# Kernel tuning notes

Measured on AMD Instinct MI355X. Metric: run time of the kernel, lower is better.

The kernel has to match this reference:

```python
import jax, jax.numpy as jnp
import numpy as np

NUM_EXPERTS = 8
TOP_K = 2


def setup_inputs() -> dict:
    key = jax.random.key(0)
    k1, k2, k3, k4, k5 = jax.random.split(key, 5)
    B, S, H, F, E = 4, 2048, 1024, 4096, NUM_EXPERTS
    return {
        "hidden_states": jax.random.normal(k1, (B, S, H), dtype=jnp.float32),
        "gate_w": jax.random.normal(k2, (E, H), dtype=jnp.float32) * 0.02,
        "w1": jax.random.normal(k3, (E, F, H), dtype=jnp.float32) * 0.02,
        "w3": jax.random.normal(k4, (E, F, H), dtype=jnp.float32) * 0.02,
        "w2": jax.random.normal(k5, (E, H, F), dtype=jnp.float32) * 0.02,
    }


def reference(hidden_states, gate_w, w1, w3, w2):
    B, S, H = hidden_states.shape
    E = gate_w.shape[0]
    x = hidden_states.reshape(-1, H)  # [T, H]
    T = x.shape[0]

    # Router: logits -> fp32 softmax -> top-k -> renormalize (Mixtral)
    router_logits = x @ gate_w.T  # [T, E]
    probs = jax.nn.softmax(router_logits.astype(jnp.float32), axis=-1)
    top_w, top_idx = jax.lax.top_k(probs, TOP_K)  # [T, K]
    top_w = top_w / jnp.sum(top_w, axis=-1, keepdims=True)
    top_w = top_w.astype(x.dtype)

    # Combine weights per (token, expert); zero for unselected experts.
    comb = jnp.zeros((T, E), dtype=x.dtype).at[
        jnp.arange(T)[:, None], top_idx
    ].add(top_w)  # [T, E]

    out = jnp.zeros((T, H), dtype=x.dtype)
    for e in range(E):  # structural loop over distinct expert weights
        h = jax.nn.silu(x @ w1[e].T) * (x @ w3[e].T)  # [T, F]
        out = out + comb[:, e:e + 1] * (h @ w2[e].T)  # [T, H]

    return out.reshape(B, S, H), router_logits
```

## Files before the change

kernel.cpp:

```cpp
#include <hip/hip_runtime.h>
#include <hip/hip_bf16.h>
#include <stdint.h>

#define T_TOK 8192
#define H_DIM 1024
#define F_DIM 4096
#define NEXP  8
#define CAP        17408
#define CAP_TILES  136

typedef __attribute__((ext_vector_type(8))) short bf16x8;
typedef __attribute__((ext_vector_type(4))) float f32x4;

#define AS1 __attribute__((address_space(1)))
#define AS3 __attribute__((address_space(3)))

__device__ __forceinline__ void gload_lds16(const void* g, void* l) {
  __builtin_amdgcn_global_load_lds((const AS1 void*)g, (AS3 void*)l, 16, 0, 0);
}

struct TK { int i0, i1; float w0, w1; };

__global__ __launch_bounds__(256) void router_kernel(
    const float* __restrict__ x, const float* __restrict__ gw,
    float* __restrict__ logits, int* __restrict__ counts, TK* __restrict__ tk)
{
  const int lane = threadIdx.x & 63;
  const int t = blockIdx.x * 4 + (threadIdx.x >> 6);
  const float* xp = x + (size_t)t * H_DIM;
  float xr[16];
#pragma unroll
  for (int i = 0; i < 16; ++i) xr[i] = xp[lane + i * 64];
  float lg[NEXP];
#pragma unroll
  for (int e = 0; e < NEXP; ++e) {
    const float* gp = gw + e * H_DIM;
    float acc = 0.f;
#pragma unroll
    for (int i = 0; i < 16; ++i) acc += xr[i] * gp[lane + i * 64];
#pragma unroll
    for (int s = 32; s > 0; s >>= 1) acc += __shfl_xor(acc, s, 64);
    lg[e] = acc;
  }
  if (lane < NEXP) logits[(size_t)t * NEXP + lane] = lg[lane];
  if (lane == 0) {
    int i0 = 0; float m0 = lg[0];
#pragma unroll
    for (int e = 1; e < NEXP; ++e) if (lg[e] > m0) { m0 = lg[e]; i0 = e; }
    int i1 = -1; float m1 = -1e30f;
#pragma unroll
    for (int e = 0; e < NEXP; ++e) if (e != i0 && lg[e] > m1) { m1 = lg[e]; i1 = e; }
    float r = expf(m1 - m0);
    float w0 = 1.f / (1.f + r);
    float w1 = r / (1.f + r);
    TK v; v.i0 = i0; v.i1 = i1; v.w0 = w0; v.w1 = w1;
    tk[t] = v;
    atomicAdd(&counts[i0], 1);
    atomicAdd(&counts[i1], 1);
  }
}

__global__ void scan_kernel(const int* __restrict__ counts, int* __restrict__ offs,
                            int* __restrict__ cursor, int* __restrict__ tile_expert)
{
  if (threadIdx.x == 0 && blockIdx.x == 0) {
    int o = 0;
    for (int e = 0; e < NEXP; ++e) {
      offs[e] = o; cursor[e] = o;
      o += (counts[e] + 127) & ~127;
    }
    offs[NEXP] = o;
    for (int ti = 0; ti < CAP_TILES; ++ti) {
      int row = ti * 128;
      int e = NEXP - 1;
      for (int k = 0; k < NEXP; ++k)
        if (row >= offs[k] && row < offs[k + 1]) { e = k; break; }
      tile_expert[ti] = e;
    }
  }
}

__global__ __launch_bounds__(256) void scatter_kernel(
    const TK* __restrict__ tk, int* __restrict__ cursor,
    int* __restrict__ pair_tok, float* __restrict__ pair_w)
{
  int t = blockIdx.x * 256 + threadIdx.x;
  if (t >= T_TOK) return;
  TK v = tk[t];
  int p0 = atomicAdd(&cursor[v.i0], 1);
  pair_tok[p0] = t; pair_w[p0] = v.w0;
  int p1 = atomicAdd(&cursor[v.i1], 1);
  pair_tok[p1] = t; pair_w[p1] = v.w1;
}

union Pack8 { __hip_bfloat16 o[8]; uint4 u; };

__global__ __launch_bounds__(256) void gather_kernel(
    const float* __restrict__ x, const int* __restrict__ pair_tok,
    __hip_bfloat16* __restrict__ xg)
{
  int idx = blockIdx.x * 256 + threadIdx.x;
  int row = idx >> 7;
  int c8  = (idx & 127) << 3;
  int tok = pair_tok[row];
  const float4* src = reinterpret_cast<const float4*>(x + (size_t)tok * H_DIM + c8);
  float4 a = src[0], b = src[1];
  Pack8 pk;
  pk.o[0] = __float2bfloat16(a.x); pk.o[1] = __float2bfloat16(a.y);
  pk.o[2] = __float2bfloat16(a.z); pk.o[3] = __float2bfloat16(a.w);
  pk.o[4] = __float2bfloat16(b.x); pk.o[5] = __float2bfloat16(b.y);
  pk.o[6] = __float2bfloat16(b.z); pk.o[7] = __float2bfloat16(b.w);
  *reinterpret_cast<uint4*>(xg + (size_t)row * H_DIM + c8) = pk.u;
}

__global__ __launch_bounds__(256) void convert_kernel(
    const float* __restrict__ src, __hip_bfloat16* __restrict__ dst, long long n)
{
  long long i = ((long long)blockIdx.x * 256 + threadIdx.x) * 8;
  if (i >= n) return;
  float4 a = *reinterpret_cast<const float4*>(src + i);
  float4 b = *reinterpret_cast<const float4*>(src + i + 4);
  Pack8 pk;
  pk.o[0] = __float2bfloat16(a.x); pk.o[1] = __float2bfloat16(a.y);
  pk.o[2] = __float2bfloat16(a.z); pk.o[3] = __float2bfloat16(a.w);
  pk.o[4] = __float2bfloat16(b.x); pk.o[5] = __float2bfloat16(b.y);
  pk.o[6] = __float2bfloat16(b.z); pk.o[7] = __float2bfloat16(b.w);
  *reinterpret_cast<uint4*>(dst + i) = pk.u;
}

__global__ __launch_bounds__(256, 2) void gemm1_kernel(
    const __hip_bfloat16* __restrict__ xg,
    const __hip_bfloat16* __restrict__ w1b,
    const __hip_bfloat16* __restrict__ w3b,
    const int* __restrict__ tile_expert,
    __hip_bfloat16* __restrict__ h)
{
  __shared__ __hip_bfloat16 sA[128 * 32], sB1[128 * 32], sB3[128 * 32];
  const int tm = blockIdx.x;
  const int tf = blockIdx.y;
  const int e  = tile_expert[tm];
  const int tid = threadIdx.x;

  const __hip_bfloat16* A  = xg  + (size_t)tm * 128 * H_DIM;
  const __hip_bfloat16* B1 = w1b + (size_t)e * F_DIM * H_DIM + (size_t)tf * 128 * H_DIM;
  const __hip_bfloat16* B3 = w3b + (size_t)e * F_DIM * H_DIM + (size_t)tf * 128 * H_DIM;

  const int r   = tid >> 2;
  const int kc  = (tid & 3) * 8;
  const int lo  = tid * 8;

  f32x4 acc1[4][4] = {};
  f32x4 acc3[4][4] = {};

  const int wv = tid >> 6, lane = tid & 63;
  const int wr = wv >> 1, wc = wv & 1;
  const int l16 = lane & 15, lk = lane >> 4;

  for (int kt = 0; kt < H_DIM / 32; ++kt) {
    __syncthreads();
    const int gk = kt * 32 + kc;
    gload_lds16(A  + (size_t)r * H_DIM + gk,          &sA [lo]);
    gload_lds16(A  + (size_t)(r + 64) * H_DIM + gk,   &sA [2048 + lo]);
    gload_lds16(B1 + (size_t)r * H_DIM + gk,          &sB1[lo]);
    gload_lds16(B1 + (size_t)(r + 64) * H_DIM + gk,   &sB1[2048 + lo]);
    gload_lds16(B3 + (size_t)r * H_DIM + gk,          &sB3[lo]);
    gload_lds16(B3 + (size_t)(r + 64) * H_DIM + gk,   &sB3[2048 + lo]);
    __syncthreads();

    bf16x8 af[4], b1f[4], b3f[4];
#pragma unroll
    for (int m = 0; m < 4; ++m)
      af[m] = *reinterpret_cast<const bf16x8*>(&sA[(wr * 64 + m * 16 + l16) * 32 + lk * 8]);
#pragma unroll
    for (int n = 0; n < 4; ++n) {
      b1f[n] = *reinterpret_cast<const bf16x8*>(&sB1[(wc * 64 + n * 16 + l16) * 32 + lk * 8]);
      b3f[n] = *reinterpret_cast<const bf16x8*>(&sB3[(wc * 64 + n * 16 + l16) * 32 + lk * 8]);
    }
#pragma unroll
    for (int m = 0; m < 4; ++m)
#pragma unroll
      for (int n = 0; n < 4; ++n) {
        acc1[m][n] = __builtin_amdgcn_mfma_f32_16x16x32_bf16(af[m], b1f[n], acc1[m][n], 0, 0, 0);
        acc3[m][n] = __builtin_amdgcn_mfma_f32_16x16x32_bf16(af[m], b3f[n], acc3[m][n], 0, 0, 0);
      }
  }

  __hip_bfloat16* hp = h + (size_t)tm * 128 * F_DIM + (size_t)tf * 128;
#pragma unroll
  for (int m = 0; m < 4; ++m)
#pragma unroll
    for (int n = 0; n < 4; ++n)
#pragma unroll
      for (int j = 0; j < 4; ++j) {
        int row = wr * 64 + m * 16 + lk * 4 + j;
        int col = wc * 64 + n * 16 + l16;
        float c1 = acc1[m][n][j];
        float c3 = acc3[m][n][j];
        float s  = c1 / (1.f + expf(-c1));
        hp[(size_t)row * F_DIM + col] = __float2bfloat16(s * c3);
      }
}

__global__ __launch_bounds__(256) void gemm2_kernel(
    const __hip_bfloat16* __restrict__ h,
    const __hip_bfloat16* __restrict__ w2b,
    const int* __restrict__ tile_expert,
    const int* __restrict__ pair_tok,
    const float* __restrict__ pair_w,
    float* __restrict__ out)
{
  __shared__ __hip_bfloat16 sA[128 * 32], sB[128 * 32];
  const int tm = blockIdx.x;
  const int tn = blockIdx.y;
  const int e  = tile_expert[tm];
  const int tid = threadIdx.x;

  const __hip_bfloat16* A = h   + (size_t)tm * 128 * F_DIM;
  const __hip_bfloat16* B = w2b + (size_t)e * H_DIM * F_DIM + (size_t)tn * 128 * F_DIM;

  const int r  = tid >> 2;
  const int kc = (tid & 3) * 8;
  const int lo = tid * 8;

  f32x4 acc[4][4] = {};
  const int wv = tid >> 6, lane = tid & 63;
  const int wr = wv >> 1, wc = wv & 1;
  const int l16 = lane & 15, lk = lane >> 4;

  for (int kt = 0; kt < F_DIM / 32; ++kt) {
    __syncthreads();
    const int gk = kt * 32 + kc;
    gload_lds16(A + (size_t)r * F_DIM + gk,          &sA[lo]);
    gload_lds16(A + (size_t)(r + 64) * F_DIM + gk,   &sA[2048 + lo]);
    gload_lds16(B + (size_t)r * F_DIM + gk,          &sB[lo]);
    gload_lds16(B + (size_t)(r + 64) * F_DIM + gk,   &sB[2048 + lo]);
    __syncthreads();

    bf16x8 af[4], bf[4];
#pragma unroll
    for (int m = 0; m < 4; ++m)
      af[m] = *reinterpret_cast<const bf16x8*>(&sA[(wr * 64 + m * 16 + l16) * 32 + lk * 8]);
#pragma unroll
    for (int n = 0; n < 4; ++n)
      bf[n] = *reinterpret_cast<const bf16x8*>(&sB[(wc * 64 + n * 16 + l16) * 32 + lk * 8]);
#pragma unroll
    for (int m = 0; m < 4; ++m)
#pragma unroll
      for (int n = 0; n < 4; ++n)
        acc[m][n] = __builtin_amdgcn_mfma_f32_16x16x32_bf16(af[m], bf[n], acc[m][n], 0, 0, 0);
  }

#pragma unroll
  for (int m = 0; m < 4; ++m)
#pragma unroll
    for (int j = 0; j < 4; ++j) {
      int rowg = tm * 128 + wr * 64 + m * 16 + lk * 4 + j;
      float w = pair_w[rowg];
      if (w != 0.f) {
        int tok = pair_tok[rowg];
        float* op = out + (size_t)tok * H_DIM + tn * 128 + wc * 64;
#pragma unroll
        for (int n = 0; n < 4; ++n)
          atomicAdd(op + n * 16 + l16, w * acc[m][n][j]);
      }
    }
}

#define WS_COUNTS   0
#define WS_CURSOR   32
#define WS_OFFS     64
#define WS_TILEEXP  128
#define WS_TK       1024
#define WS_PAIRTOK  132096
#define WS_PAIRW    201728
#define WS_ZERO_BYTES 271360
#define WS_XG       271872ll
#define WS_W1       (WS_XG + 35651584ll)
#define WS_W3       (WS_W1 + 67108864ll)
#define WS_W2       (WS_W3 + 67108864ll)
#define WS_H        (WS_W2 + 67108864ll)

extern "C" void kernel_launch(void* const* d_in, const int* in_sizes, int n_in,
                              void* d_out, int out_size, void* d_ws, size_t ws_size,
                              hipStream_t stream) {
  const float* x  = (const float*)d_in[0];
  const float* gw = (const float*)d_in[1];
  const float* w1 = (const float*)d_in[2];
  const float* w3 = (const float*)d_in[3];
  const float* w2 = (const float*)d_in[4];
  float* out    = (float*)d_out;
  float* logits = out + (size_t)T_TOK * H_DIM;

  char* ws = (char*)d_ws;
  int*   counts   = (int*)(ws + WS_COUNTS);
  int*   cursor   = (int*)(ws + WS_CURSOR);
  int*   offs     = (int*)(ws + WS_OFFS);
  int*   tile_exp = (int*)(ws + WS_TILEEXP);
  TK*    tk       = (TK*)(ws + WS_TK);
  int*   pair_tok = (int*)(ws + WS_PAIRTOK);
  float* pair_w   = (float*)(ws + WS_PAIRW);
  __hip_bfloat16* xg  = (__hip_bfloat16*)(ws + WS_XG);
  __hip_bfloat16* w1b = (__hip_bfloat16*)(ws + WS_W1);
  __hip_bfloat16* w3b = (__hip_bfloat16*)(ws + WS_W3);
  __hip_bfloat16* w2b = (__hip_bfloat16*)(ws + WS_W2);
  __hip_bfloat16* hbuf = (__hip_bfloat16*)(ws + WS_H);

  hipMemsetAsync(d_ws, 0, WS_ZERO_BYTES, stream);
  hipMemsetAsync(d_out, 0, (size_t)T_TOK * H_DIM * sizeof(float), stream);

  const long long nW = (long long)NEXP * F_DIM * H_DIM;
  convert_kernel<<<16384, 256, 0, stream>>>(w1, w1b, nW);
  convert_kernel<<<16384, 256, 0, stream>>>(w3, w3b, nW);
  convert_kernel<<<16384, 256, 0, stream>>>(w2, w2b, nW);

  router_kernel<<<T_TOK / 4, 256, 0, stream>>>(x, gw, logits, counts, tk);
  scan_kernel<<<1, 64, 0, stream>>>(counts, offs, cursor, tile_exp);
  scatter_kernel<<<T_TOK / 256, 256, 0, stream>>>(tk, cursor, pair_tok, pair_w);
  gather_kernel<<<(CAP * 128) / 256, 256, 0, stream>>>(x, pair_tok, xg);

  gemm1_kernel<<<dim3(CAP_TILES, F_DIM / 128), 256, 0, stream>>>(
      xg, w1b, w3b, tile_exp, hbuf);
  gemm2_kernel<<<dim3(CAP_TILES, H_DIM / 128), 256, 0, stream>>>(
      hbuf, w2b, tile_exp, pair_tok, pair_w, out);
}
```

Baseline: 1.068 ms.

## Swizzle LDS, remap block order, replace atomic scatter with combine kernel

Applies an XOR swizzle to the LDS tile layout in both GEMMs to cut bank conflicts on the fragment reads. Remaps the flattened block index so consecutive blocks share weight tiles, improving L2 reuse. gemm2 now writes weighted per-pair rows to a dense fp32 buffer instead of issuing atomicAdds, and a new combine kernel sums each token's two rows using an inverse index built during scatter. This also drops the output memset and parallelises the tile-expert lookup in the scan kernel. The cost is an extra fp32 intermediate of about 71 MB that is written and read back, which overwrites xg after gemm1 has finished with it.

```diff
diff --git a/kernel.cpp b/kernel.cpp
--- a/kernel.cpp
+++ b/kernel.cpp
@@ -60,29 +60,35 @@
   }
 }
 
-__global__ void scan_kernel(const int* __restrict__ counts, int* __restrict__ offs,
-                            int* __restrict__ cursor, int* __restrict__ tile_expert)
-{
-  if (threadIdx.x == 0 && blockIdx.x == 0) {
+__global__ __launch_bounds__(256) void scan_kernel(
+    const int* __restrict__ counts, int* __restrict__ offs,
+    int* __restrict__ cursor, int* __restrict__ tile_expert)
+{
+  __shared__ int so[NEXP + 1];
+  const int tid = threadIdx.x;
+  if (tid == 0) {
     int o = 0;
     for (int e = 0; e < NEXP; ++e) {
-      offs[e] = o; cursor[e] = o;
+      so[e] = o; offs[e] = o; cursor[e] = o;
       o += (counts[e] + 127) & ~127;
     }
-    offs[NEXP] = o;
-    for (int ti = 0; ti < CAP_TILES; ++ti) {
-      int row = ti * 128;
-      int e = NEXP - 1;
-      for (int k = 0; k < NEXP; ++k)
-        if (row >= offs[k] && row < offs[k + 1]) { e = k; break; }
-      tile_expert[ti] = e;
-    }
+    so[NEXP] = o; offs[NEXP] = o;
+  }
+  __syncthreads();
+  for (int ti = tid; ti < CAP_TILES; ti += 256) {
+    int row = ti * 128;
+    int e = NEXP - 1;
+#pragma unroll
+    for (int k = 0; k < NEXP; ++k)
+      if (row >= so[k] && row < so[k + 1]) { e = k; break; }
+    tile_expert[ti] = e;
   }
 }
 
 __global__ __launch_bounds__(256) void scatter_kernel(
     const TK* __restrict__ tk, int* __restrict__ cursor,
-    int* __restrict__ pair_tok, float* __restrict__ pair_w)
+    int* __restrict__ pair_tok, float* __restrict__ pair_w,
+    int2* __restrict__ inv)
 {
   int t = blockIdx.x * 256 + threadIdx.x;
   if (t >= T_TOK) return;
@@ -91,6 +97,7 @@
   pair_tok[p0] = t; pair_w[p0] = v.w0;
   int p1 = atomicAdd(&cursor[v.i1], 1);
   pair_tok[p1] = t; pair_w[p1] = v.w1;
+  inv[t] = make_int2(p0, p1);
 }
 
 union Pack8 { __hip_bfloat16 o[8]; uint4 u; };
@@ -128,6 +135,7 @@
   *reinterpret_cast<uint4*>(dst + i) = pk.u;
 }
 
+
 __global__ __launch_bounds__(256, 2) void gemm1_kernel(
     const __hip_bfloat16* __restrict__ xg,
     const __hip_bfloat16* __restrict__ w1b,
@@ -136,8 +144,10 @@
     __hip_bfloat16* __restrict__ h)
 {
   __shared__ __hip_bfloat16 sA[128 * 32], sB1[128 * 32], sB3[128 * 32];
-  const int tm = blockIdx.x;
-  const int tf = blockIdx.y;
+  const int n_ = blockIdx.x;
+  const int swz = (n_ & 7) * 544 + (n_ >> 3);
+  const int tf = swz & 31;
+  const int tm = swz >> 5;
   const int e  = tile_expert[tm];
   const int tid = threadIdx.x;
 
@@ -145,9 +155,10 @@
   const __hip_bfloat16* B1 = w1b + (size_t)e * F_DIM * H_DIM + (size_t)tf * 128 * H_DIM;
   const __hip_bfloat16* B3 = w3b + (size_t)e * F_DIM * H_DIM + (size_t)tf * 128 * H_DIM;
 
-  const int r   = tid >> 2;
-  const int kc  = (tid & 3) * 8;
-  const int lo  = tid * 8;
+  const int r     = tid >> 2;
+  const int s_src = (tid & 3) ^ ((r >> 1) & 3);
+  const int kc    = s_src * 8;
+  const int lo    = tid * 8;
 
   f32x4 acc1[4][4] = {};
   f32x4 acc3[4][4] = {};
@@ -155,6 +166,7 @@
   const int wv = tid >> 6, lane = tid & 63;
   const int wr = wv >> 1, wc = wv & 1;
   const int l16 = lane & 15, lk = lane >> 4;
+  const int rdk = (lk * 8) ^ (((l16 >> 1) & 3) * 8);
 
   for (int kt = 0; kt < H_DIM / 32; ++kt) {
     __syncthreads();
@@ -170,11 +182,11 @@
     bf16x8 af[4], b1f[4], b3f[4];
 #pragma unroll
     for (int m = 0; m < 4; ++m)
-      af[m] = *reinterpret_cast<const bf16x8*>(&sA[(wr * 64 + m * 16 + l16) * 32 + lk * 8]);
+      af[m] = *reinterpret_cast<const bf16x8*>(&sA[(wr * 64 + m * 16 + l16) * 32 + rdk]);
 #pragma unroll
     for (int n = 0; n < 4; ++n) {
-      b1f[n] = *reinterpret_cast<const bf16x8*>(&sB1[(wc * 64 + n * 16 + l16) * 32 + lk * 8]);
-      b3f[n] = *reinterpret_cast<const bf16x8*>(&sB3[(wc * 64 + n * 16 + l16) * 32 + lk * 8]);
+      b1f[n] = *reinterpret_cast<const bf16x8*>(&sB1[(wc * 64 + n * 16 + l16) * 32 + rdk]);
+      b3f[n] = *reinterpret_cast<const bf16x8*>(&sB3[(wc * 64 + n * 16 + l16) * 32 + rdk]);
     }
 #pragma unroll
     for (int m = 0; m < 4; ++m)
@@ -201,31 +213,34 @@
       }
 }
 
-__global__ __launch_bounds__(256) void gemm2_kernel(
+__global__ __launch_bounds__(256, 2) void gemm2_kernel(
     const __hip_bfloat16* __restrict__ h,
     const __hip_bfloat16* __restrict__ w2b,
     const int* __restrict__ tile_expert,
-    const int* __restrict__ pair_tok,
     const float* __restrict__ pair_w,
-    float* __restrict__ out)
+    float* __restrict__ y)
 {
   __shared__ __hip_bfloat16 sA[128 * 32], sB[128 * 32];
-  const int tm = blockIdx.x;
-  const int tn = blockIdx.y;
+  const int n_ = blockIdx.x;
+  const int swz = (n_ & 7) * 136 + (n_ >> 3);
+  const int tn = swz & 7;
+  const int tm = swz >> 3;
   const int e  = tile_expert[tm];
   const int tid = threadIdx.x;
 
   const __hip_bfloat16* A = h   + (size_t)tm * 128 * F_DIM;
   const __hip_bfloat16* B = w2b + (size_t)e * H_DIM * F_DIM + (size_t)tn * 128 * F_DIM;
 
-  const int r  = tid >> 2;
-  const int kc = (tid & 3) * 8;
-  const int lo = tid * 8;
+  const int r     = tid >> 2;
+  const int s_src = (tid & 3) ^ ((r >> 1) & 3);
+  const int kc    = s_src * 8;
+  const int lo    = tid * 8;
 
   f32x4 acc[4][4] = {};
   const int wv = tid >> 6, lane = tid & 63;
   const int wr = wv >> 1, wc = wv & 1;
   const int l16 = lane & 15, lk = lane >> 4;
+  const int rdk = (lk * 8) ^ (((l16 >> 1) & 3) * 8);
 
   for (int kt = 0; kt < F_DIM / 32; ++kt) {
     __syncthreads();
@@ -239,10 +254,10 @@
     bf16x8 af[4], bf[4];
 #pragma unroll
     for (int m = 0; m < 4; ++m)
-      af[m] = *reinterpret_cast<const bf16x8*>(&sA[(wr * 64 + m * 16 + l16) * 32 + lk * 8]);
+      af[m] = *reinterpret_cast<const bf16x8*>(&sA[(wr * 64 + m * 16 + l16) * 32 + rdk]);
 #pragma unroll
     for (int n = 0; n < 4; ++n)
-      bf[n] = *reinterpret_cast<const bf16x8*>(&sB[(wc * 64 + n * 16 + l16) * 32 + lk * 8]);
+      bf[n] = *reinterpret_cast<const bf16x8*>(&sB[(wc * 64 + n * 16 + l16) * 32 + rdk]);
 #pragma unroll
     for (int m = 0; m < 4; ++m)
 #pragma unroll
@@ -256,14 +271,25 @@
     for (int j = 0; j < 4; ++j) {
       int rowg = tm * 128 + wr * 64 + m * 16 + lk * 4 + j;
       float w = pair_w[rowg];
-      if (w != 0.f) {
-        int tok = pair_tok[rowg];
-        float* op = out + (size_t)tok * H_DIM + tn * 128 + wc * 64;
-#pragma unroll
-        for (int n = 0; n < 4; ++n)
-          atomicAdd(op + n * 16 + l16, w * acc[m][n][j]);
-      }
+      float* op = y + (size_t)rowg * H_DIM + tn * 128 + wc * 64;
+#pragma unroll
+      for (int n = 0; n < 4; ++n)
+        op[n * 16 + l16] = w * acc[m][n][j];
     }
+}
+
+__global__ __launch_bounds__(256) void combine_kernel(
+    const float* __restrict__ y, const int2* __restrict__ inv,
+    float* __restrict__ out)
+{
+  int idx = blockIdx.x * 256 + threadIdx.x;
+  int t  = idx >> 8;
+  int c  = (idx & 255) << 2;
+  int2 p = inv[t];
+  float4 a = *reinterpret_cast<const float4*>(y + (size_t)p.x * H_DIM + c);
+  float4 b = *reinterpret_cast<const float4*>(y + (size_t)p.y * H_DIM + c);
+  float4 o; o.x = a.x + b.x; o.y = a.y + b.y; o.z = a.z + b.z; o.w = a.w + b.w;
+  *reinterpret_cast<float4*>(out + (size_t)t * H_DIM + c) = o;
 }
 
 #define WS_COUNTS   0
@@ -274,11 +300,13 @@
 #define WS_PAIRTOK  132096
 #define WS_PAIRW    201728
 #define WS_ZERO_BYTES 271360
-#define WS_XG       271872ll
+#define WS_INV      271360
+#define WS_XG       336896ll
 #define WS_W1       (WS_XG + 35651584ll)
 #define WS_W3       (WS_W1 + 67108864ll)
 #define WS_W2       (WS_W3 + 67108864ll)
 #define WS_H        (WS_W2 + 67108864ll)
+#define WS_Y        WS_XG
 
 extern "C" void kernel_launch(void* const* d_in, const int* in_sizes, int n_in,
                               void* d_out, int out_size, void* d_ws, size_t ws_size,
@@ -299,14 +327,15 @@
   TK*    tk       = (TK*)(ws + WS_TK);
   int*   pair_tok = (int*)(ws + WS_PAIRTOK);
   float* pair_w   = (float*)(ws + WS_PAIRW);
+  int2*  inv      = (int2*)(ws + WS_INV);
   __hip_bfloat16* xg  = (__hip_bfloat16*)(ws + WS_XG);
   __hip_bfloat16* w1b = (__hip_bfloat16*)(ws + WS_W1);
   __hip_bfloat16* w3b = (__hip_bfloat16*)(ws + WS_W3);
   __hip_bfloat16* w2b = (__hip_bfloat16*)(ws + WS_W2);
   __hip_bfloat16* hbuf = (__hip_bfloat16*)(ws + WS_H);
+  float* ybuf = (float*)(ws + WS_Y);
 
   hipMemsetAsync(d_ws, 0, WS_ZERO_BYTES, stream);
-  hipMemsetAsync(d_out, 0, (size_t)T_TOK * H_DIM * sizeof(float), stream);
 
   const long long nW = (long long)NEXP * F_DIM * H_DIM;
   convert_kernel<<<16384, 256, 0, stream>>>(w1, w1b, nW);
@@ -314,12 +343,13 @@
   convert_kernel<<<16384, 256, 0, stream>>>(w2, w2b, nW);
 
   router_kernel<<<T_TOK / 4, 256, 0, stream>>>(x, gw, logits, counts, tk);
-  scan_kernel<<<1, 64, 0, stream>>>(counts, offs, cursor, tile_exp);
-  scatter_kernel<<<T_TOK / 256, 256, 0, stream>>>(tk, cursor, pair_tok, pair_w);
+  scan_kernel<<<1, 256, 0, stream>>>(counts, offs, cursor, tile_exp);
+  scatter_kernel<<<T_TOK / 256, 256, 0, stream>>>(tk, cursor, pair_tok, pair_w, inv);
   gather_kernel<<<(CAP * 128) / 256, 256, 0, stream>>>(x, pair_tok, xg);
 
-  gemm1_kernel<<<dim3(CAP_TILES, F_DIM / 128), 256, 0, stream>>>(
+  gemm1_kernel<<<CAP_TILES * (F_DIM / 128), 256, 0, stream>>>(
       xg, w1b, w3b, tile_exp, hbuf);
-  gemm2_kernel<<<dim3(CAP_TILES, H_DIM / 128), 256, 0, stream>>>(
-      hbuf, w2b, tile_exp, pair_tok, pair_w, out);
-}
+  gemm2_kernel<<<CAP_TILES * (H_DIM / 128), 256, 0, stream>>>(
+      hbuf, w2b, tile_exp, pair_w, ybuf);
+  combine_kernel<<<(T_TOK * H_DIM / 4) / 256, 256, 0, stream>>>(ybuf, inv, out);
+}
```

Result: faster. 1.011 ms (-5.4%).
